# Kernel tuning notes

Measured on AMD Instinct MI355X. Metric: run time of the kernel, lower is better.

## Reference

```python
import jax, jax.numpy as jnp
import numpy as np

H = 51      # hidden_size
IN = 1      # input_size
T = 512     # timesteps
B = 1024    # batch


def setup_inputs() -> dict:
    key = jax.random.key(0)
    ks = jax.random.split(key, 11)
    s = 1.0 / np.sqrt(H)  # PyTorch default init scale for LSTMCell/Linear
    u = lambda k, shape: jax.random.uniform(k, shape, jnp.float32, -s, s)
    return {
        "input": jax.random.normal(ks[0], (T, B, IN), jnp.float32),
        "W_ih1": u(ks[1], (4 * H, IN)),
        "W_hh1": u(ks[2], (4 * H, H)),
        "b_ih1": u(ks[3], (4 * H,)),
        "b_hh1": u(ks[4], (4 * H,)),
        "W_ih2": u(ks[5], (4 * H, H)),
        "W_hh2": u(ks[6], (4 * H, H)),
        "b_ih2": u(ks[7], (4 * H,)),
        "b_hh2": u(ks[8], (4 * H,)),
        "W_lin": u(ks[9], (1, H)),
        "b_lin": u(ks[10], (1,)),
        "future": 0,
    }


def _cell(x, h, c, W_ih, W_hh, b_ih, b_hh):
    # PyTorch LSTMCell: gates ordered (i, f, g, o)
    gates = x @ W_ih.T + h @ W_hh.T + (b_ih + b_hh)  # (B, 4H)
    i, f, g, o = jnp.split(gates, 4, axis=-1)
    c_new = jax.nn.sigmoid(f) * c + jax.nn.sigmoid(i) * jnp.tanh(g)
    h_new = jax.nn.sigmoid(o) * jnp.tanh(c_new)
    return h_new, c_new


def reference(input, W_ih1, W_hh1, b_ih1, b_hh1,
              W_ih2, W_hh2, b_ih2, b_hh2, W_lin, b_lin, future):
    n = input.shape[1]
    z = jnp.zeros((n, H), input.dtype)

    def step(carry, x_t):
        h1, c1, h2, c2 = carry
        h1, c1 = _cell(x_t, h1, c1, W_ih1, W_hh1, b_ih1, b_hh1)
        h2, c2 = _cell(h1, h2, c2, W_ih2, W_hh2, b_ih2, b_hh2)
        out = h2 @ W_lin.T + b_lin  # (B, 1)
        return (h1, c1, h2, c2), out

    carry, outs = jax.lax.scan(step, (z, z, z, z), input)  # outs: (T, B, 1)

    if future > 0:  # static Python int -> static branch
        def fstep(carry, _):
            h1, c1, h2, c2, out = carry
            h1, c1 = _cell(out, h1, c1, W_ih1, W_hh1, b_ih1, b_hh1)
            h2, c2 = _cell(h1, h2, c2, W_ih2, W_hh2, b_ih2, b_hh2)
            out = h2 @ W_lin.T + b_lin
            return (h1, c1, h2, c2, out), out

        h1, c1, h2, c2 = carry
        _, fouts = jax.lax.scan(fstep, (h1, c1, h2, c2, outs[-1]), None,
                                length=future)
        outs = jnp.concatenate([outs, fouts], axis=0)

    # torch cat(dim=1) of (B,1) slices -> (B, T+future)
    return outs[..., 0].T
```

## Files before the change

kernel.cpp:

```cpp
#include <hip/hip_runtime.h>


#define Hs   51
#define HP   52
#define G4   204
#define Ts   512
#define Bs   1024
#define NB   4
#define NT   768

__device__ __forceinline__ float sig_(float x) {
    return 1.0f / (1.0f + __expf(-x));
}
__device__ __forceinline__ float tanh_(float x) {
    float e = __expf(2.0f * x);
    return 1.0f - 2.0f / (e + 1.0f);
}

#define MATVEC4(HBASE, A0, A1, A2, A3)                                        \
    {                                                                         \
        const float4* p0_ = (const float4*)((HBASE));                         \
        const float4* p1_ = (const float4*)((HBASE) + HP);                    \
        const float4* p2_ = (const float4*)((HBASE) + 2 * HP);                \
        const float4* p3_ = (const float4*)((HBASE) + 3 * HP);                \
        _Pragma("unroll")                                                     \
        for (int k_ = 0; k_ < HP / 4; ++k_) {                                 \
            float4 v0_ = p0_[k_], v1_ = p1_[k_], v2_ = p2_[k_], v3_ = p3_[k_];\
            float w0_ = w[4 * k_ + 0], w1_ = w[4 * k_ + 1];                   \
            float w2_ = w[4 * k_ + 2], w3_ = w[4 * k_ + 3];                   \
            A0 = fmaf(w0_, v0_.x, A0); A0 = fmaf(w1_, v0_.y, A0);             \
            A0 = fmaf(w2_, v0_.z, A0); A0 = fmaf(w3_, v0_.w, A0);             \
            A1 = fmaf(w0_, v1_.x, A1); A1 = fmaf(w1_, v1_.y, A1);             \
            A1 = fmaf(w2_, v1_.z, A1); A1 = fmaf(w3_, v1_.w, A1);             \
            A2 = fmaf(w0_, v2_.x, A2); A2 = fmaf(w1_, v2_.y, A2);             \
            A2 = fmaf(w2_, v2_.z, A2); A2 = fmaf(w3_, v2_.w, A2);             \
            A3 = fmaf(w0_, v3_.x, A3); A3 = fmaf(w1_, v3_.y, A3);             \
            A3 = fmaf(w2_, v3_.z, A3); A3 = fmaf(w3_, v3_.w, A3);             \
        }                                                                     \
    }

__global__ __launch_bounds__(NT, 3) void lstm2_kernel(
    const float* __restrict__ x,
    const float* __restrict__ W_ih1,
    const float* __restrict__ W_hh1,
    const float* __restrict__ b_ih1,
    const float* __restrict__ b_hh1,
    const float* __restrict__ W_ih2,
    const float* __restrict__ W_hh2,
    const float* __restrict__ b_ih2,
    const float* __restrict__ b_hh2,
    const float* __restrict__ W_lin,
    const float* __restrict__ b_lin,
    float* __restrict__ out)
{
    __shared__ __align__(16) float xs[Ts][NB];
    __shared__ __align__(16) float h1b[2][NB][HP];
    __shared__ __align__(16) float h2b[2][NB][HP];
    __shared__ __align__(16) float g1[NB][G4];
    __shared__ __align__(16) float g2a[NB][G4];
    __shared__ __align__(16) float g2b[NB][G4];
    __shared__ __align__(16) float wlin_s[HP];
    __shared__ float blin_s;

    const int tid = threadIdx.x;
    const int bg0 = blockIdx.x * NB;

    for (int idx = tid; idx < Ts * NB; idx += NT) {
        int tt = idx >> 2;
        int b  = idx & 3;
        xs[tt][b] = x[tt * Bs + bg0 + b];
    }
    if (tid < 2 * NB * HP) {
        ((float*)h1b)[tid] = 0.f;
        ((float*)h2b)[tid] = 0.f;
    }
    if (tid < HP) wlin_s[tid] = (tid < Hs) ? W_lin[tid] : 0.f;
    if (tid == 0) blin_s = b_lin[0];

    float w[HP];
    float bsum = 0.f, wih1 = 0.f;
    if (tid < G4) {
        const float* src = W_hh1 + tid * Hs;
        #pragma unroll
        for (int k = 0; k < Hs; ++k) w[k] = src[k];
        w[Hs] = 0.f;
        bsum = b_ih1[tid] + b_hh1[tid];
        wih1 = W_ih1[tid];
    } else if (tid >= 256 && tid < 256 + G4) {
        const int r = tid - 256;
        const float* src = W_ih2 + r * Hs;
        #pragma unroll
        for (int k = 0; k < Hs; ++k) w[k] = src[k];
        w[Hs] = 0.f;
        bsum = b_ih2[r] + b_hh2[r];
    } else if (tid >= 512 && tid < 512 + G4) {
        const int r = tid - 512;
        const float* src = W_hh2 + r * Hs;
        #pragma unroll
        for (int k = 0; k < Hs; ++k) w[k] = src[k];
        w[Hs] = 0.f;
    }

    int eb = 0, ej = 0;
    if (tid < G4) { eb = tid / Hs; ej = tid - eb * Hs; }
    else if (tid >= 256 && tid < 256 + G4) {
        const int r = tid - 256; eb = r / Hs; ej = r - eb * Hs;
    }

    float cc = 0.f;
    __syncthreads();

    for (int it = 0; it <= Ts; ++it) {
        if (tid < G4) {
            if (it < Ts) {
                const int pr = (it - 1) & 1;
                const float4 xv = *(const float4*)xs[it];
                float a0 = fmaf(wih1, xv.x, bsum);
                float a1 = fmaf(wih1, xv.y, bsum);
                float a2 = fmaf(wih1, xv.z, bsum);
                float a3 = fmaf(wih1, xv.w, bsum);
                MATVEC4(&h1b[pr][0][0], a0, a1, a2, a3);
                g1[0][tid] = a0; g1[1][tid] = a1;
                g1[2][tid] = a2; g1[3][tid] = a3;
            }
        } else if (tid < G4 + NB) {
            if (it >= 2) {
                const int b = tid - G4;
                const float4* hb = (const float4*)h2b[it & 1][b];
                const float4* wv = (const float4*)wlin_s;
                float s = blin_s;
                #pragma unroll
                for (int k = 0; k < HP / 4; ++k) {
                    float4 a = hb[k], ww = wv[k];
                    s += a.x * ww.x + a.y * ww.y + a.z * ww.z + a.w * ww.w;
                }
                out[(bg0 + b) * Ts + (it - 2)] = s;
            }
        } else if (tid >= 256 && tid < 256 + G4) {
            if (it >= 1) {
                const int r  = tid - 256;
                const int pr = (it - 1) & 1;
                float a0 = bsum, a1 = bsum, a2 = bsum, a3 = bsum;
                MATVEC4(&h1b[pr][0][0], a0, a1, a2, a3);
                g2a[0][r] = a0; g2a[1][r] = a1;
                g2a[2][r] = a2; g2a[3][r] = a3;
            }
        } else if (tid >= 512 && tid < 512 + G4) {
            if (it >= 1) {
                const int r  = tid - 512;
                const int pr = it & 1;
                float a0 = 0.f, a1 = 0.f, a2 = 0.f, a3 = 0.f;
                MATVEC4(&h2b[pr][0][0], a0, a1, a2, a3);
                g2b[0][r] = a0; g2b[1][r] = a1;
                g2b[2][r] = a2; g2b[3][r] = a3;
            }
        }
        __syncthreads();

        if (tid < G4) {
            if (it < Ts) {
                float iv = sig_ (g1[eb][ej]);
                float fv = sig_ (g1[eb][Hs + ej]);
                float gv = tanh_(g1[eb][2 * Hs + ej]);
                float ov = sig_ (g1[eb][3 * Hs + ej]);
                cc = fmaf(fv, cc, iv * gv);
                h1b[it & 1][eb][ej] = ov * tanh_(cc);
            }
        } else if (tid >= 256 && tid < 256 + G4) {
            if (it >= 1) {
                float s0 = g2a[eb][ej]          + g2b[eb][ej];
                float s1 = g2a[eb][Hs + ej]     + g2b[eb][Hs + ej];
                float s2 = g2a[eb][2 * Hs + ej] + g2b[eb][2 * Hs + ej];
                float s3 = g2a[eb][3 * Hs + ej] + g2b[eb][3 * Hs + ej];
                float iv = sig_(s0);
                float fv = sig_(s1);
                float gv = tanh_(s2);
                float ov = sig_(s3);
                cc = fmaf(fv, cc, iv * gv);
                h2b[(it - 1) & 1][eb][ej] = ov * tanh_(cc);
            }
        }
        __syncthreads();
    }

    if (tid >= G4 && tid < G4 + NB) {
        const int b = tid - G4;
        const float4* hb = (const float4*)h2b[(Ts - 1) & 1][b];
        const float4* wv = (const float4*)wlin_s;
        float s = blin_s;
        #pragma unroll
        for (int k = 0; k < HP / 4; ++k) {
            float4 a = hb[k], ww = wv[k];
            s += a.x * ww.x + a.y * ww.y + a.z * ww.z + a.w * ww.w;
        }
        out[(bg0 + b) * Ts + (Ts - 1)] = s;
    }
}

extern "C" void kernel_launch(void* const* d_in, const int* in_sizes, int n_in,
                              void* d_out, int out_size, void* d_ws, size_t ws_size,
                              hipStream_t stream) {
    const float* x     = (const float*)d_in[0];
    const float* W_ih1 = (const float*)d_in[1];
    const float* W_hh1 = (const float*)d_in[2];
    const float* b_ih1 = (const float*)d_in[3];
    const float* b_hh1 = (const float*)d_in[4];
    const float* W_ih2 = (const float*)d_in[5];
    const float* W_hh2 = (const float*)d_in[6];
    const float* b_ih2 = (const float*)d_in[7];
    const float* b_hh2 = (const float*)d_in[8];
    const float* W_lin = (const float*)d_in[9];
    const float* b_lin = (const float*)d_in[10];
    float* out = (float*)d_out;

    lstm2_kernel<<<Bs / NB, NT, 0, stream>>>(
        x, W_ih1, W_hh1, b_ih1, b_hh1,
        W_ih2, W_hh2, b_ih2, b_hh2, W_lin, b_lin, out);
}
```

Baseline: 1.135 ms.

## Broadcast hidden state via readlane and split batch across wave pairs

Replaces the per-thread LDS float4 reads of the hidden-state vectors with one LDS load per lane, followed by __builtin_amdgcn_readlane broadcasts inside the matvec. Work is reorganised so each wave pair handles two batch rows, and each thread computes two gate rows (r and r+102) for those two batches. This removes most LDS read traffic from the inner loop in exchange for scalar readlane instructions and roughly double the per-thread weight registers (two 51-float rows), which could raise register pressure and cause spills under the 768-thread launch bounds.

```diff
diff --git a/kernel.cpp b/kernel.cpp
--- a/kernel.cpp
+++ b/kernel.cpp
@@ -16,28 +16,9 @@
     float e = __expf(2.0f * x);
     return 1.0f - 2.0f / (e + 1.0f);
 }
-
-#define MATVEC4(HBASE, A0, A1, A2, A3)                                        \
-    {                                                                         \
-        const float4* p0_ = (const float4*)((HBASE));                         \
-        const float4* p1_ = (const float4*)((HBASE) + HP);                    \
-        const float4* p2_ = (const float4*)((HBASE) + 2 * HP);                \
-        const float4* p3_ = (const float4*)((HBASE) + 3 * HP);                \
-        _Pragma("unroll")                                                     \
-        for (int k_ = 0; k_ < HP / 4; ++k_) {                                 \
-            float4 v0_ = p0_[k_], v1_ = p1_[k_], v2_ = p2_[k_], v3_ = p3_[k_];\
-            float w0_ = w[4 * k_ + 0], w1_ = w[4 * k_ + 1];                   \
-            float w2_ = w[4 * k_ + 2], w3_ = w[4 * k_ + 3];                   \
-            A0 = fmaf(w0_, v0_.x, A0); A0 = fmaf(w1_, v0_.y, A0);             \
-            A0 = fmaf(w2_, v0_.z, A0); A0 = fmaf(w3_, v0_.w, A0);             \
-            A1 = fmaf(w0_, v1_.x, A1); A1 = fmaf(w1_, v1_.y, A1);             \
-            A1 = fmaf(w2_, v1_.z, A1); A1 = fmaf(w3_, v1_.w, A1);             \
-            A2 = fmaf(w0_, v2_.x, A2); A2 = fmaf(w1_, v2_.y, A2);             \
-            A2 = fmaf(w2_, v2_.z, A2); A2 = fmaf(w3_, v2_.w, A2);             \
-            A3 = fmaf(w0_, v3_.x, A3); A3 = fmaf(w1_, v3_.y, A3);             \
-            A3 = fmaf(w2_, v3_.z, A3); A3 = fmaf(w3_, v3_.w, A3);             \
-        }                                                                     \
-    }
+__device__ __forceinline__ float bcast_(float v, int k) {
+    return __int_as_float(__builtin_amdgcn_readlane(__float_as_int(v), k));
+}
 
 __global__ __launch_bounds__(NT, 3) void lstm2_kernel(
     const float* __restrict__ x,
@@ -54,146 +35,186 @@
     float* __restrict__ out)
 {
     __shared__ __align__(16) float xs[Ts][NB];
-    __shared__ __align__(16) float h1b[2][NB][HP];
-    __shared__ __align__(16) float h2b[2][NB][HP];
-    __shared__ __align__(16) float g1[NB][G4];
+    __shared__ __align__(16) float h1b_[2][NB][HP];
+    __shared__ __align__(16) float h2b_[2][NB][HP];
+    __shared__ __align__(16) float g1 [NB][G4];
     __shared__ __align__(16) float g2a[NB][G4];
     __shared__ __align__(16) float g2b[NB][G4];
     __shared__ __align__(16) float wlin_s[HP];
     __shared__ float blin_s;
 
-    const int tid = threadIdx.x;
-    const int bg0 = blockIdx.x * NB;
+    const int tid  = threadIdx.x;
+    const int lane = tid & 63;
+    const int wv   = tid >> 6;
+    const int role = wv >> 2;
+    const int lw   = wv & 3;
+    const int g    = lw >> 1;
+    const int rp   = ((lw & 1) << 6) + lane;
+    const bool mv  = rp < 102;
+    const int b0   = 2 * g, b1 = b0 + 1;
+    const int bg0  = blockIdx.x * NB;
 
     for (int idx = tid; idx < Ts * NB; idx += NT) {
-        int tt = idx >> 2;
-        int b  = idx & 3;
+        int tt = idx >> 2, b = idx & 3;
         xs[tt][b] = x[tt * Bs + bg0 + b];
     }
     if (tid < 2 * NB * HP) {
-        ((float*)h1b)[tid] = 0.f;
-        ((float*)h2b)[tid] = 0.f;
+        ((float*)h1b_)[tid] = 0.f;
+        ((float*)h2b_)[tid] = 0.f;
     }
     if (tid < HP) wlin_s[tid] = (tid < Hs) ? W_lin[tid] : 0.f;
     if (tid == 0) blin_s = b_lin[0];
 
-    float w[HP];
-    float bsum = 0.f, wih1 = 0.f;
-    if (tid < G4) {
-        const float* src = W_hh1 + tid * Hs;
+    float wA[Hs], wB[Hs];
+    float bsA = 0.f, bsB = 0.f, wihA = 0.f, wihB = 0.f;
+    if (mv) {
+        const int r0 = rp, r1 = rp + 102;
+        const float* M = (role == 0) ? W_hh1 : (role == 1) ? W_ih2 : W_hh2;
         #pragma unroll
-        for (int k = 0; k < Hs; ++k) w[k] = src[k];
-        w[Hs] = 0.f;
-        bsum = b_ih1[tid] + b_hh1[tid];
-        wih1 = W_ih1[tid];
-    } else if (tid >= 256 && tid < 256 + G4) {
-        const int r = tid - 256;
-        const float* src = W_ih2 + r * Hs;
-        #pragma unroll
-        for (int k = 0; k < Hs; ++k) w[k] = src[k];
-        w[Hs] = 0.f;
-        bsum = b_ih2[r] + b_hh2[r];
-    } else if (tid >= 512 && tid < 512 + G4) {
-        const int r = tid - 512;
-        const float* src = W_hh2 + r * Hs;
-        #pragma unroll
-        for (int k = 0; k < Hs; ++k) w[k] = src[k];
-        w[Hs] = 0.f;
+        for (int k = 0; k < Hs; ++k) {
+            wA[k] = M[r0 * Hs + k];
+            wB[k] = M[r1 * Hs + k];
+        }
+        if (role == 0) {
+            bsA = b_ih1[r0] + b_hh1[r0];
+            bsB = b_ih1[r1] + b_hh1[r1];
+            wihA = W_ih1[r0];
+            wihB = W_ih1[r1];
+        } else if (role == 1) {
+            bsA = b_ih2[r0] + b_hh2[r0];
+            bsB = b_ih2[r1] + b_hh2[r1];
+        }
     }
 
     int eb = 0, ej = 0;
-    if (tid < G4) { eb = tid / Hs; ej = tid - eb * Hs; }
-    else if (tid >= 256 && tid < 256 + G4) {
-        const int r = tid - 256; eb = r / Hs; ej = r - eb * Hs;
-    }
+    if (mv && role < 2) {
+        int c = g * 102 + rp;
+        eb = c / 51;
+        ej = c - eb * 51;
+    }
+    const bool isOut = (wv == 11) && (lane >= 40) && (lane < 44);
+    const int  ob    = lane - 40;
 
     float cc = 0.f;
     __syncthreads();
 
     for (int it = 0; it <= Ts; ++it) {
-        if (tid < G4) {
-            if (it < Ts) {
-                const int pr = (it - 1) & 1;
-                const float4 xv = *(const float4*)xs[it];
-                float a0 = fmaf(wih1, xv.x, bsum);
-                float a1 = fmaf(wih1, xv.y, bsum);
-                float a2 = fmaf(wih1, xv.z, bsum);
-                float a3 = fmaf(wih1, xv.w, bsum);
-                MATVEC4(&h1b[pr][0][0], a0, a1, a2, a3);
-                g1[0][tid] = a0; g1[1][tid] = a1;
-                g1[2][tid] = a2; g1[3][tid] = a3;
-            }
-        } else if (tid < G4 + NB) {
-            if (it >= 2) {
-                const int b = tid - G4;
-                const float4* hb = (const float4*)h2b[it & 1][b];
-                const float4* wv = (const float4*)wlin_s;
+        const int pr1 = (it - 1) & 1;
+        const int pr2 = it & 1;
+
+        float h1A = 0.f, h1B = 0.f, h2A = 0.f, h2B = 0.f;
+        if (lane < HP) {
+            h1A = h1b_[pr1][b0][lane];
+            h1B = h1b_[pr1][b1][lane];
+            h2A = h2b_[pr2][b0][lane];
+            h2B = h2b_[pr2][b1][lane];
+        }
+
+        if (role == 0) {
+            if (mv && it < Ts) {
+                float xv0 = xs[it][b0], xv1 = xs[it][b1];
+                float aA0 = fmaf(wihA, xv0, bsA);
+                float aB0 = fmaf(wihB, xv0, bsB);
+                float aA1 = fmaf(wihA, xv1, bsA);
+                float aB1 = fmaf(wihB, xv1, bsB);
+                #pragma unroll
+                for (int k = 0; k < Hs; ++k) {
+                    float ha = bcast_(h1A, k);
+                    float hb = bcast_(h1B, k);
+                    aA0 = fmaf(wA[k], ha, aA0);
+                    aB0 = fmaf(wB[k], ha, aB0);
+                    aA1 = fmaf(wA[k], hb, aA1);
+                    aB1 = fmaf(wB[k], hb, aB1);
+                }
+                g1[b0][rp]       = aA0;
+                g1[b0][rp + 102] = aB0;
+                g1[b1][rp]       = aA1;
+                g1[b1][rp + 102] = aB1;
+            }
+        } else if (role == 1) {
+            if (mv && it >= 1) {
+                float aA0 = bsA, aB0 = bsB, aA1 = bsA, aB1 = bsB;
+                #pragma unroll
+                for (int k = 0; k < Hs; ++k) {
+                    float ha = bcast_(h1A, k);
+                    float hb = bcast_(h1B, k);
+                    aA0 = fmaf(wA[k], ha, aA0);
+                    aB0 = fmaf(wB[k], ha, aB0);
+                    aA1 = fmaf(wA[k], hb, aA1);
+                    aB1 = fmaf(wB[k], hb, aB1);
+                }
+                g2a[b0][rp]       = aA0;
+                g2a[b0][rp + 102] = aB0;
+                g2a[b1][rp]       = aA1;
+                g2a[b1][rp + 102] = aB1;
+            }
+        } else {
+            if (mv && it >= 1) {
+                float aA0 = 0.f, aB0 = 0.f, aA1 = 0.f, aB1 = 0.f;
+                #pragma unroll
+                for (int k = 0; k < Hs; ++k) {
+                    float ha = bcast_(h2A, k);
+                    float hb = bcast_(h2B, k);
+                    aA0 = fmaf(wA[k], ha, aA0);
+                    aB0 = fmaf(wB[k], ha, aB0);
+                    aA1 = fmaf(wA[k], hb, aA1);
+                    aB1 = fmaf(wB[k], hb, aB1);
+                }
+                g2b[b0][rp]       = aA0;
+                g2b[b0][rp + 102] = aB0;
+                g2b[b1][rp]       = aA1;
+                g2b[b1][rp + 102] = aB1;
+            }
+            if (isOut && it >= 2) {
+                const float4* hb4 = (const float4*)h2b_[pr2][ob];
+                const float4* wv4 = (const float4*)wlin_s;
                 float s = blin_s;
                 #pragma unroll
                 for (int k = 0; k < HP / 4; ++k) {
-                    float4 a = hb[k], ww = wv[k];
-                    s += a.x * ww.x + a.y * ww.y + a.z * ww.z + a.w * ww.w;
-                }
-                out[(bg0 + b) * Ts + (it - 2)] = s;
-            }
-        } else if (tid >= 256 && tid < 256 + G4) {
-            if (it >= 1) {
-                const int r  = tid - 256;
-                const int pr = (it - 1) & 1;
-                float a0 = bsum, a1 = bsum, a2 = bsum, a3 = bsum;
-                MATVEC4(&h1b[pr][0][0], a0, a1, a2, a3);
-                g2a[0][r] = a0; g2a[1][r] = a1;
-                g2a[2][r] = a2; g2a[3][r] = a3;
-            }
-        } else if (tid >= 512 && tid < 512 + G4) {
-            if (it >= 1) {
-                const int r  = tid - 512;
-                const int pr = it & 1;
-                float a0 = 0.f, a1 = 0.f, a2 = 0.f, a3 = 0.f;
-                MATVEC4(&h2b[pr][0][0], a0, a1, a2, a3);
-                g2b[0][r] = a0; g2b[1][r] = a1;
-                g2b[2][r] = a2; g2b[3][r] = a3;
+                    float4 a = hb4[k], w = wv4[k];
+                    s += a.x * w.x + a.y * w.y + a.z * w.z + a.w * w.w;
+                }
+                out[(bg0 + ob) * Ts + (it - 2)] = s;
             }
         }
         __syncthreads();
 
-        if (tid < G4) {
+        if (mv && role == 0) {
             if (it < Ts) {
                 float iv = sig_ (g1[eb][ej]);
-                float fv = sig_ (g1[eb][Hs + ej]);
-                float gv = tanh_(g1[eb][2 * Hs + ej]);
-                float ov = sig_ (g1[eb][3 * Hs + ej]);
+                float fv = sig_ (g1[eb][ej + Hs]);
+                float gv = tanh_(g1[eb][ej + 2 * Hs]);
+                float ov = sig_ (g1[eb][ej + 3 * Hs]);
                 cc = fmaf(fv, cc, iv * gv);
-                h1b[it & 1][eb][ej] = ov * tanh_(cc);
-            }
-        } else if (tid >= 256 && tid < 256 + G4) {
+                h1b_[it & 1][eb][ej] = ov * tanh_(cc);
+            }
+        } else if (mv && role == 1) {
             if (it >= 1) {
                 float s0 = g2a[eb][ej]          + g2b[eb][ej];
-                float s1 = g2a[eb][Hs + ej]     + g2b[eb][Hs + ej];
-                float s2 = g2a[eb][2 * Hs + ej] + g2b[eb][2 * Hs + ej];
-                float s3 = g2a[eb][3 * Hs + ej] + g2b[eb][3 * Hs + ej];
+                float s1 = g2a[eb][ej + Hs]     + g2b[eb][ej + Hs];
+                float s2 = g2a[eb][ej + 2 * Hs] + g2b[eb][ej + 2 * Hs];
+                float s3 = g2a[eb][ej + 3 * Hs] + g2b[eb][ej + 3 * Hs];
                 float iv = sig_(s0);
                 float fv = sig_(s1);
                 float gv = tanh_(s2);
                 float ov = sig_(s3);
                 cc = fmaf(fv, cc, iv * gv);
-                h2b[(it - 1) & 1][eb][ej] = ov * tanh_(cc);
+                h2b_[(it - 1) & 1][eb][ej] = ov * tanh_(cc);
             }
         }
         __syncthreads();
     }
 
-    if (tid >= G4 && tid < G4 + NB) {
-        const int b = tid - G4;
-        const float4* hb = (const float4*)h2b[(Ts - 1) & 1][b];
-        const float4* wv = (const float4*)wlin_s;
+    if (isOut) {
+        const float4* hb4 = (const float4*)h2b_[(Ts - 1) & 1][ob];
+        const float4* wv4 = (const float4*)wlin_s;
         float s = blin_s;
         #pragma unroll
         for (int k = 0; k < HP / 4; ++k) {
-            float4 a = hb[k], ww = wv[k];
-            s += a.x * ww.x + a.y * ww.y + a.z * ww.z + a.w * ww.w;
-        }
-        out[(bg0 + b) * Ts + (Ts - 1)] = s;
+            float4 a = hb4[k], w = wv4[k];
+            s += a.x * w.x + a.y * w.y + a.z * w.z + a.w * w.w;
+        }
+        out[(bg0 + ob) * Ts + (Ts - 1)] = s;
     }
 }
 
```

Measured after the change: 1.394 ms. 22.8% more time.

## Compute LSTM gate matvecs with bf16x3 MFMA on 256-thread blocks

Applied to the files above, without the earlier changes.

Replaces the per-thread FP32 register matvecs with MFMA 16x16x32 bf16 instructions. Weights and hidden states are split into high and low bf16 parts, and four products are summed so the result stays close to fp32. The block shrinks from 768 to 256 threads, and the two layer-2 matvecs are merged into one K=102 product over concatenated [h1,h2] operands. This is meant to cut the per-step FMA instruction count on the serial recurrence. The cost is extra split/convert work, more MFMAs per tile, and sequential MFMA dependency chains on the critical path.

```diff
diff --git a/kernel.cpp b/kernel.cpp
--- a/kernel.cpp
+++ b/kernel.cpp
@@ -2,44 +2,28 @@
 
 
 #define Hs   51
-#define HP   52
 #define G4   204
 #define Ts   512
 #define Bs   1024
 #define NB   4
-#define NT   768
-
-__device__ __forceinline__ float sig_(float x) {
-    return 1.0f / (1.0f + __expf(-x));
-}
-__device__ __forceinline__ float tanh_(float x) {
-    float e = __expf(2.0f * x);
-    return 1.0f - 2.0f / (e + 1.0f);
-}
-
-#define MATVEC4(HBASE, A0, A1, A2, A3)                                        \
-    {                                                                         \
-        const float4* p0_ = (const float4*)((HBASE));                         \
-        const float4* p1_ = (const float4*)((HBASE) + HP);                    \
-        const float4* p2_ = (const float4*)((HBASE) + 2 * HP);                \
-        const float4* p3_ = (const float4*)((HBASE) + 3 * HP);                \
-        _Pragma("unroll")                                                     \
-        for (int k_ = 0; k_ < HP / 4; ++k_) {                                 \
-            float4 v0_ = p0_[k_], v1_ = p1_[k_], v2_ = p2_[k_], v3_ = p3_[k_];\
-            float w0_ = w[4 * k_ + 0], w1_ = w[4 * k_ + 1];                   \
-            float w2_ = w[4 * k_ + 2], w3_ = w[4 * k_ + 3];                   \
-            A0 = fmaf(w0_, v0_.x, A0); A0 = fmaf(w1_, v0_.y, A0);             \
-            A0 = fmaf(w2_, v0_.z, A0); A0 = fmaf(w3_, v0_.w, A0);             \
-            A1 = fmaf(w0_, v1_.x, A1); A1 = fmaf(w1_, v1_.y, A1);             \
-            A1 = fmaf(w2_, v1_.z, A1); A1 = fmaf(w3_, v1_.w, A1);             \
-            A2 = fmaf(w0_, v2_.x, A2); A2 = fmaf(w1_, v2_.y, A2);             \
-            A2 = fmaf(w2_, v2_.z, A2); A2 = fmaf(w3_, v2_.w, A2);             \
-            A3 = fmaf(w0_, v3_.x, A3); A3 = fmaf(w1_, v3_.y, A3);             \
-            A3 = fmaf(w2_, v3_.z, A3); A3 = fmaf(w3_, v3_.w, A3);             \
-        }                                                                     \
-    }
-
-__global__ __launch_bounds__(NT, 3) void lstm2_kernel(
+#define NT   256
+#define S1   72
+#define S2   136
+
+typedef __attribute__((ext_vector_type(8))) short  bf16x8;
+typedef __attribute__((ext_vector_type(4))) float  f32x4;
+
+__device__ __forceinline__ float sig_(float x)  { return 1.0f / (1.0f + __expf(-x)); }
+__device__ __forceinline__ float tanh_(float x) { float e = __expf(2.0f * x); return 1.0f - 2.0f / (e + 1.0f); }
+__device__ __forceinline__ unsigned short bfh_(float x) {
+    unsigned u = __float_as_uint(x);
+    return (unsigned short)((u + 0x7FFFu + ((u >> 16) & 1u)) >> 16);
+}
+__device__ __forceinline__ float bff_(unsigned short h) {
+    return __uint_as_float(((unsigned)h) << 16);
+}
+
+__global__ __launch_bounds__(NT, 1) void lstm2_kernel(
     const float* __restrict__ x,
     const float* __restrict__ W_ih1,
     const float* __restrict__ W_hh1,
@@ -53,145 +37,206 @@
     const float* __restrict__ b_lin,
     float* __restrict__ out)
 {
-    __shared__ __align__(16) float xs[Ts][NB];
-    __shared__ __align__(16) float h1b[2][NB][HP];
-    __shared__ __align__(16) float h2b[2][NB][HP];
-    __shared__ __align__(16) float g1[NB][G4];
-    __shared__ __align__(16) float g2a[NB][G4];
-    __shared__ __align__(16) float g2b[NB][G4];
-    __shared__ __align__(16) float wlin_s[HP];
+    __shared__ __align__(16) float  xs[Ts][NB];
+    __shared__ __align__(16) unsigned short a1h[16 * S1];
+    __shared__ __align__(16) unsigned short a1l[16 * S1];
+    __shared__ __align__(16) unsigned short a2h[16 * S2];
+    __shared__ __align__(16) unsigned short a2l[16 * S2];
+    __shared__ __align__(16) float  g1s[NB][208];
+    __shared__ __align__(16) float  g2s[NB][208];
+    __shared__ __align__(16) float  h2f[NB][52];
+    __shared__ __align__(16) float  wlin_s[52];
     __shared__ float blin_s;
 
-    const int tid = threadIdx.x;
-    const int bg0 = blockIdx.x * NB;
-
-    for (int idx = tid; idx < Ts * NB; idx += NT) {
-        int tt = idx >> 2;
-        int b  = idx & 3;
+    const int tid  = threadIdx.x;
+    const int lane = tid & 63;
+    const int wv   = tid >> 6;
+    const int m    = lane & 15;
+    const int ch   = lane >> 4;
+    const int nT   = (wv == 0) ? 4 : 3;
+    const int bg0  = blockIdx.x * NB;
+
+    for (int i = tid; i < Ts * NB; i += NT) {
+        int tt = i >> 2, b = i & 3;
         xs[tt][b] = x[tt * Bs + bg0 + b];
     }
-    if (tid < 2 * NB * HP) {
-        ((float*)h1b)[tid] = 0.f;
-        ((float*)h2b)[tid] = 0.f;
-    }
-    if (tid < HP) wlin_s[tid] = (tid < Hs) ? W_lin[tid] : 0.f;
+    for (int i = tid; i < 16 * S1; i += NT) { a1h[i] = 0; a1l[i] = 0; }
+    for (int i = tid; i < 16 * S2; i += NT) { a2h[i] = 0; a2l[i] = 0; }
+    for (int i = tid; i < NB * 52; i += NT) ((float*)h2f)[i] = 0.f;
+    if (tid < 52) wlin_s[tid] = (tid < Hs) ? W_lin[tid] : 0.f;
     if (tid == 0) blin_s = b_lin[0];
-
-    float w[HP];
-    float bsum = 0.f, wih1 = 0.f;
-    if (tid < G4) {
-        const float* src = W_hh1 + tid * Hs;
-        #pragma unroll
-        for (int k = 0; k < Hs; ++k) w[k] = src[k];
-        w[Hs] = 0.f;
-        bsum = b_ih1[tid] + b_hh1[tid];
-        wih1 = W_ih1[tid];
-    } else if (tid >= 256 && tid < 256 + G4) {
-        const int r = tid - 256;
-        const float* src = W_ih2 + r * Hs;
-        #pragma unroll
-        for (int k = 0; k < Hs; ++k) w[k] = src[k];
-        w[Hs] = 0.f;
-        bsum = b_ih2[r] + b_hh2[r];
-    } else if (tid >= 512 && tid < 512 + G4) {
-        const int r = tid - 512;
-        const float* src = W_hh2 + r * Hs;
-        #pragma unroll
-        for (int k = 0; k < Hs; ++k) w[k] = src[k];
-        w[Hs] = 0.f;
-    }
-
-    int eb = 0, ej = 0;
-    if (tid < G4) { eb = tid / Hs; ej = tid - eb * Hs; }
-    else if (tid >= 256 && tid < 256 + G4) {
-        const int r = tid - 256; eb = r / Hs; ej = r - eb * Hs;
-    }
-
-    float cc = 0.f;
+    if (tid >= 208 && tid < 212) {
+        int b = tid - 208;
+        float xv = x[0 * Bs + bg0 + b];
+        unsigned short hh = bfh_(xv);
+        a1h[b * S1 + Hs] = hh;
+        a1l[b * S1 + Hs] = bfh_(xv - bff_(hh));
+    }
+
+    bf16x8 B1h[4][2], B1l[4][2];
+    bf16x8 B2h[4][4], B2l[4][4];
+    float  bias1f[4], bias2f[4];
+    #pragma unroll
+    for (int i = 0; i < 4; ++i) {
+        if (i >= nT) continue;
+        const int t = (i < 3) ? (wv + 4 * i) : 12;
+        const int r = t * 16 + m;
+        bias1f[i] = (r < G4) ? (b_ih1[r] + b_hh1[r]) : 0.f;
+        bias2f[i] = (r < G4) ? (b_ih2[r] + b_hh2[r]) : 0.f;
+        #pragma unroll
+        for (int s = 0; s < 2; ++s) {
+            bf16x8 h8, l8;
+            #pragma unroll
+            for (int j = 0; j < 8; ++j) {
+                const int k = s * 32 + ch * 8 + j;
+                float v = 0.f;
+                if (r < G4) {
+                    if (k < Hs)       v = W_hh1[r * Hs + k];
+                    else if (k == Hs) v = W_ih1[r];
+                }
+                unsigned short hh = bfh_(v);
+                h8[j] = (short)hh;
+                l8[j] = (short)bfh_(v - bff_(hh));
+            }
+            B1h[i][s] = h8; B1l[i][s] = l8;
+        }
+        #pragma unroll
+        for (int s = 0; s < 4; ++s) {
+            bf16x8 h8, l8;
+            #pragma unroll
+            for (int j = 0; j < 8; ++j) {
+                const int k = s * 32 + ch * 8 + j;
+                float v = 0.f;
+                if (r < G4) {
+                    if (k < Hs)          v = W_ih2[r * Hs + k];
+                    else if (k < 2 * Hs) v = W_hh2[r * Hs + (k - Hs)];
+                }
+                unsigned short hh = bfh_(v);
+                h8[j] = (short)hh;
+                l8[j] = (short)bfh_(v - bff_(hh));
+            }
+            B2h[i][s] = h8; B2l[i][s] = l8;
+        }
+    }
+
+    float c1 = 0.f, c2 = 0.f;
     __syncthreads();
 
     for (int it = 0; it <= Ts; ++it) {
+        bf16x8 A1h_[2], A1l_[2], A2h_[4], A2l_[4];
+        if (it < Ts) {
+            #pragma unroll
+            for (int s = 0; s < 2; ++s) {
+                A1h_[s] = *(const bf16x8*)&a1h[m * S1 + s * 32 + ch * 8];
+                A1l_[s] = *(const bf16x8*)&a1l[m * S1 + s * 32 + ch * 8];
+            }
+        }
+        if (it >= 1) {
+            #pragma unroll
+            for (int s = 0; s < 4; ++s) {
+                A2h_[s] = *(const bf16x8*)&a2h[m * S2 + s * 32 + ch * 8];
+                A2l_[s] = *(const bf16x8*)&a2l[m * S2 + s * 32 + ch * 8];
+            }
+        }
+
+        f32x4 acc1[4], acc2[4];
+        #pragma unroll
+        for (int i = 0; i < 4; ++i) {
+            if (i >= nT) continue;
+            if (it < Ts) {
+                f32x4 a = {bias1f[i], bias1f[i], bias1f[i], bias1f[i]};
+                #pragma unroll
+                for (int s = 0; s < 2; ++s) {
+                    a = __builtin_amdgcn_mfma_f32_16x16x32_bf16(A1h_[s], B1h[i][s], a, 0, 0, 0);
+                    a = __builtin_amdgcn_mfma_f32_16x16x32_bf16(A1l_[s], B1h[i][s], a, 0, 0, 0);
+                    a = __builtin_amdgcn_mfma_f32_16x16x32_bf16(A1h_[s], B1l[i][s], a, 0, 0, 0);
+                    a = __builtin_amdgcn_mfma_f32_16x16x32_bf16(A1l_[s], B1l[i][s], a, 0, 0, 0);
+                }
+                acc1[i] = a;
+            }
+            if (it >= 1) {
+                f32x4 a = {bias2f[i], bias2f[i], bias2f[i], bias2f[i]};
+                #pragma unroll
+                for (int s = 0; s < 4; ++s) {
+                    a = __builtin_amdgcn_mfma_f32_16x16x32_bf16(A2h_[s], B2h[i][s], a, 0, 0, 0);
+                    a = __builtin_amdgcn_mfma_f32_16x16x32_bf16(A2l_[s], B2h[i][s], a, 0, 0, 0);
+                    a = __builtin_amdgcn_mfma_f32_16x16x32_bf16(A2h_[s], B2l[i][s], a, 0, 0, 0);
+                    a = __builtin_amdgcn_mfma_f32_16x16x32_bf16(A2l_[s], B2l[i][s], a, 0, 0, 0);
+                }
+                acc2[i] = a;
+            }
+        }
+        if (lane < 16) {
+            #pragma unroll
+            for (int i = 0; i < 4; ++i) {
+                if (i >= nT) continue;
+                const int t   = (i < 3) ? (wv + 4 * i) : 12;
+                const int col = t * 16 + m;
+                if (it < Ts) {
+                    g1s[0][col] = acc1[i].x; g1s[1][col] = acc1[i].y;
+                    g1s[2][col] = acc1[i].z; g1s[3][col] = acc1[i].w;
+                }
+                if (it >= 1) {
+                    g2s[0][col] = acc2[i].x; g2s[1][col] = acc2[i].y;
+                    g2s[2][col] = acc2[i].z; g2s[3][col] = acc2[i].w;
+                }
+            }
+        }
+        if (it >= 2 && tid >= 64 && tid < 68) {
+            const int b = tid - 64;
+            const float4* hb = (const float4*)&h2f[b][0];
+            const float4* wv4 = (const float4*)&wlin_s[0];
+            float s = blin_s;
+            #pragma unroll
+            for (int k = 0; k < 13; ++k) {
+                float4 a = hb[k], w = wv4[k];
+                s += a.x * w.x + a.y * w.y + a.z * w.z + a.w * w.w;
+            }
+            out[(bg0 + b) * Ts + (it - 2)] = s;
+        }
+        __syncthreads();
+
         if (tid < G4) {
+            const int b = tid / Hs, j = tid - b * Hs;
             if (it < Ts) {
-                const int pr = (it - 1) & 1;
-                const float4 xv = *(const float4*)xs[it];
-                float a0 = fmaf(wih1, xv.x, bsum);
-                float a1 = fmaf(wih1, xv.y, bsum);
-                float a2 = fmaf(wih1, xv.z, bsum);
-                float a3 = fmaf(wih1, xv.w, bsum);
-                MATVEC4(&h1b[pr][0][0], a0, a1, a2, a3);
-                g1[0][tid] = a0; g1[1][tid] = a1;
-                g1[2][tid] = a2; g1[3][tid] = a3;
-            }
-        } else if (tid < G4 + NB) {
-            if (it >= 2) {
-                const int b = tid - G4;
-                const float4* hb = (const float4*)h2b[it & 1][b];
-                const float4* wv = (const float4*)wlin_s;
-                float s = blin_s;
-                #pragma unroll
-                for (int k = 0; k < HP / 4; ++k) {
-                    float4 a = hb[k], ww = wv[k];
-                    s += a.x * ww.x + a.y * ww.y + a.z * ww.z + a.w * ww.w;
-                }
-                out[(bg0 + b) * Ts + (it - 2)] = s;
-            }
-        } else if (tid >= 256 && tid < 256 + G4) {
+                float gi = g1s[b][j],           gf = g1s[b][j + Hs];
+                float gg = g1s[b][j + 2 * Hs],  go = g1s[b][j + 3 * Hs];
+                c1 = fmaf(sig_(gf), c1, sig_(gi) * tanh_(gg));
+                float h1 = sig_(go) * tanh_(c1);
+                unsigned short hh = bfh_(h1);
+                unsigned short hl = bfh_(h1 - bff_(hh));
+                a1h[b * S1 + j] = hh; a1l[b * S1 + j] = hl;
+                a2h[b * S2 + j] = hh; a2l[b * S2 + j] = hl;
+            }
             if (it >= 1) {
-                const int r  = tid - 256;
-                const int pr = (it - 1) & 1;
-                float a0 = bsum, a1 = bsum, a2 = bsum, a3 = bsum;
-                MATVEC4(&h1b[pr][0][0], a0, a1, a2, a3);
-                g2a[0][r] = a0; g2a[1][r] = a1;
-                g2a[2][r] = a2; g2a[3][r] = a3;
-            }
-        } else if (tid >= 512 && tid < 512 + G4) {
-            if (it >= 1) {
-                const int r  = tid - 512;
-                const int pr = it & 1;
-                float a0 = 0.f, a1 = 0.f, a2 = 0.f, a3 = 0.f;
-                MATVEC4(&h2b[pr][0][0], a0, a1, a2, a3);
-                g2b[0][r] = a0; g2b[1][r] = a1;
-                g2b[2][r] = a2; g2b[3][r] = a3;
-            }
+                float gi = g2s[b][j],           gf = g2s[b][j + Hs];
+                float gg = g2s[b][j + 2 * Hs],  go = g2s[b][j + 3 * Hs];
+                c2 = fmaf(sig_(gf), c2, sig_(gi) * tanh_(gg));
+                float h2 = sig_(go) * tanh_(c2);
+                unsigned short hh = bfh_(h2);
+                unsigned short hl = bfh_(h2 - bff_(hh));
+                a2h[b * S2 + Hs + j] = hh; a2l[b * S2 + Hs + j] = hl;
+                h2f[b][j] = h2;
+            }
+        } else if (tid >= 208 && tid < 212 && it + 1 < Ts) {
+            const int b = tid - 208;
+            float xv = xs[it + 1][b];
+            unsigned short hh = bfh_(xv);
+            a1h[b * S1 + Hs] = hh;
+            a1l[b * S1 + Hs] = bfh_(xv - bff_(hh));
         }
         __syncthreads();
-
-        if (tid < G4) {
-            if (it < Ts) {
-                float iv = sig_ (g1[eb][ej]);
-                float fv = sig_ (g1[eb][Hs + ej]);
-                float gv = tanh_(g1[eb][2 * Hs + ej]);
-                float ov = sig_ (g1[eb][3 * Hs + ej]);
-                cc = fmaf(fv, cc, iv * gv);
-                h1b[it & 1][eb][ej] = ov * tanh_(cc);
-            }
-        } else if (tid >= 256 && tid < 256 + G4) {
-            if (it >= 1) {
-                float s0 = g2a[eb][ej]          + g2b[eb][ej];
-                float s1 = g2a[eb][Hs + ej]     + g2b[eb][Hs + ej];
-                float s2 = g2a[eb][2 * Hs + ej] + g2b[eb][2 * Hs + ej];
-                float s3 = g2a[eb][3 * Hs + ej] + g2b[eb][3 * Hs + ej];
-                float iv = sig_(s0);
-                float fv = sig_(s1);
-                float gv = tanh_(s2);
-                float ov = sig_(s3);
-                cc = fmaf(fv, cc, iv * gv);
-                h2b[(it - 1) & 1][eb][ej] = ov * tanh_(cc);
-            }
-        }
-        __syncthreads();
-    }
-
-    if (tid >= G4 && tid < G4 + NB) {
-        const int b = tid - G4;
-        const float4* hb = (const float4*)h2b[(Ts - 1) & 1][b];
-        const float4* wv = (const float4*)wlin_s;
+    }
+
+    if (tid >= 64 && tid < 68) {
+        const int b = tid - 64;
+        const float4* hb = (const float4*)&h2f[b][0];
+        const float4* wv4 = (const float4*)&wlin_s[0];
         float s = blin_s;
         #pragma unroll
-        for (int k = 0; k < HP / 4; ++k) {
-            float4 a = hb[k], ww = wv[k];
-            s += a.x * ww.x + a.y * ww.y + a.z * ww.z + a.w * ww.w;
+        for (int k = 0; k < 13; ++k) {
+            float4 a = hb[k], w = wv4[k];
+            s += a.x * w.x + a.y * w.y + a.z * w.z + a.w * w.w;
         }
         out[(bg0 + b) * Ts + (Ts - 1)] = s;
     }
```

New measurement: 1.028 ms. -9.4%, faster.
